# Kernel tuning notes

Measured on AMD Instinct MI355X. Metric: run time of the kernel, lower is better.

The kernel has to match this reference:

```python
import jax, jax.numpy as jnp
from jax import lax
import numpy as np


def _bn(x, g, b, eps=1e-5):
    # BatchNorm2d in training mode: biased batch stats over (N,H,W) per channel
    m = jnp.mean(x, axis=(0, 2, 3), keepdims=True)
    v = jnp.mean((x - m) ** 2, axis=(0, 2, 3), keepdims=True)
    return (x - m) * lax.rsqrt(v + eps) * g[None, :, None, None] + b[None, :, None, None]


def _conv(x, w, b, pad):
    y = lax.conv_general_dilated(x, w, (1, 1), [(pad, pad), (pad, pad)],
                                 dimension_numbers=('NCHW', 'OIHW', 'NCHW'))
    return y + b[None, :, None, None]


def _prelu(x, a):
    return jnp.where(x >= 0, x, a * x)


def _maxpool2(x):
    return lax.reduce_window(x, -jnp.inf, lax.max, (1, 1, 2, 2), (1, 1, 2, 2), 'VALID')


def _up2(x):
    # UpsamplingBilinear2d(scale_factor=2) -> bilinear, align_corners=True
    B, C, H, W = x.shape
    def idx(n):
        pos = jnp.arange(2 * n, dtype=x.dtype) * (n - 1) / (2 * n - 1)
        lo = jnp.floor(pos).astype(jnp.int32)
        hi = jnp.minimum(lo + 1, n - 1)
        return lo, hi, pos - lo.astype(x.dtype)
    lo, hi, f = idx(H)
    x = x[:, :, lo, :] * (1 - f)[:, None] + x[:, :, hi, :] * f[:, None]
    lo, hi, f = idx(W)
    x = x[:, :, :, lo] * (1 - f) + x[:, :, :, hi] * f
    return x


def _forward(x, n16, sigma16, bias16, prelu_a,
             bn3_g, bn3_b, bn32_g, bn32_b, bn64_g, bn64_b, bn128_g, bn128_b,
             w1, b1, w2, b2, w3, b3, w4, b4, w5, b5, w6, b6, w7, b7, w11, b11):
    B, C, H, W = x.shape
    # 16 enhancement curves fused: r_k = x^{n_k} / (x^{n_k} + sigma_k^{n_k} + bias_k)
    xn = x[None] ** n16[:, None, None, None, None]          # (16,B,3,H,W)
    r = xn / (xn + (sigma16 ** n16)[:, None, None, None, None]
              + bias16[:, None, None, None, None])
    # each branch gets its own BatchNorm2d(3) stats (same affine params)
    r = jax.vmap(lambda t: _bn(t, bn3_g, bn3_b))(r)
    x_fusion = jnp.transpose(r, (1, 0, 2, 3, 4)).reshape(B, 16 * C, H, W)
    x1 = _bn(_maxpool2(_prelu(_conv(x_fusion, w1, b1, 1), prelu_a)), bn32_g, bn32_b)
    x2 = _bn(_maxpool2(_prelu(_conv(x1, w2, b2, 1), prelu_a)), bn64_g, bn64_b)
    x3 = _bn(_maxpool2(_prelu(_conv(x2, w3, b3, 1), prelu_a)), bn128_g, bn128_b)
    x4 = _bn(_conv(x3, w4, b4, 1), bn128_g, bn128_b)
    x5 = _bn(_up2(_prelu(_conv(jnp.concatenate([x4, x3], 1), w5, b5, 1), prelu_a)), bn64_g, bn64_b)
    x6 = _bn(_up2(_prelu(_conv(jnp.concatenate([x2, x5], 1), w6, b6, 1), prelu_a)), bn32_g, bn32_b)
    x_out = jax.nn.sigmoid(_up2(_prelu(_conv(jnp.concatenate([x1, x6], 1), w7, b7, 1), prelu_a)))
    x_out = _conv(x_out, w11, b11, 0)
    x_mean = jnp.mean(x, axis=1, keepdims=True)
    x_out1 = jnp.mean(x_out, axis=1, keepdims=True)
    return x_out1 * (x / (x_mean + 1e-6))


def setup_inputs() -> dict:
    key = jax.random.key(0)
    ks = jax.random.split(key, 16)
    B, H, W = 8, 256, 256
    nf = 32
    x = jax.random.uniform(ks[0], (B, 3, H, W), jnp.float32, 1e-3, 1.0)
    n16 = jnp.arange(1, 17, dtype=jnp.float32) * 0.5
    sigma16 = jnp.full((16,), 0.5, jnp.float32)
    bias16 = jnp.full((16,), 1e-4, jnp.float32)
    prelu_a = jnp.float32(0.25)
    def cw(k, o, i, kk):
        return jax.random.normal(k, (o, i, kk, kk), jnp.float32) * 0.05
    def cb(o):
        return jnp.zeros((o,), jnp.float32)
    return dict(
        x=x, n16=n16, sigma16=sigma16, bias16=bias16, prelu_a=prelu_a,
        bn3_g=jnp.ones((3,), jnp.float32), bn3_b=jnp.zeros((3,), jnp.float32),
        bn32_g=jnp.ones((32,), jnp.float32), bn32_b=jnp.zeros((32,), jnp.float32),
        bn64_g=jnp.ones((64,), jnp.float32), bn64_b=jnp.zeros((64,), jnp.float32),
        bn128_g=jnp.ones((128,), jnp.float32), bn128_b=jnp.zeros((128,), jnp.float32),
        w1=cw(ks[1], nf, 48, 3), b1=cb(nf),
        w2=cw(ks[2], 2 * nf, nf, 3), b2=cb(2 * nf),
        w3=cw(ks[3], 4 * nf, 2 * nf, 3), b3=cb(4 * nf),
        w4=cw(ks[4], 4 * nf, 4 * nf, 3), b4=cb(4 * nf),
        w5=cw(ks[5], 2 * nf, 8 * nf, 3), b5=cb(2 * nf),
        w6=cw(ks[6], nf, 4 * nf, 3), b6=cb(nf),
        w7=cw(ks[7], nf, 2 * nf, 3), b7=cb(nf),
        w11=cw(ks[8], 3, nf, 1), b11=cb(3),
    )


def reference(x, n16, sigma16, bias16, prelu_a,
              bn3_g, bn3_b, bn32_g, bn32_b, bn64_g, bn64_b, bn128_g, bn128_b,
              w1, b1, w2, b2, w3, b3, w4, b4, w5, b5, w6, b6, w7, b7, w11, b11):
    return _forward(x, n16, sigma16, bias16, prelu_a,
                    bn3_g, bn3_b, bn32_g, bn32_b, bn64_g, bn64_b, bn128_g, bn128_b,
                    w1, b1, w2, b2, w3, b3, w4, b4, w5, b5, w6, b6, w7, b7, w11, b11)
```

## Files before the change

kernel.cpp:

```cpp
#include <hip/hip_runtime.h>

#define FAST_EXP2(x) __builtin_amdgcn_exp2f(x)
#define FAST_LOG2(x) __builtin_amdgcn_logf(x)
#define FAST_RCP(x)  __builtin_amdgcn_rcpf(x)

static constexpr size_t S3_SUM=0,   S3_SQ=48;
static constexpr size_t S32A_SUM=96,  S32A_SQ=128;
static constexpr size_t S64A_SUM=160, S64A_SQ=224;
static constexpr size_t S128A_SUM=288,S128A_SQ=416;
static constexpr size_t S128B_SUM=544,S128B_SQ=672;
static constexpr size_t S64B_SUM=800, S64B_SQ=864;
static constexpr size_t S32B_SUM=928, S32B_SQ=960;
static constexpr size_t A3_=1024,  B3_=1072;
static constexpr size_t A32A_=1120, B32A_=1152;
static constexpr size_t A64A_=1184, B64A_=1248;
static constexpr size_t A128A_=1312,B128A_=1440;
static constexpr size_t A128B_=1568,B128B_=1696;
static constexpr size_t A64B_=1824, B64B_=1888;
static constexpr size_t A32B_=1952, B32B_=1984;
static constexpr size_t SPB_=2016, WBAR_=2032, BBAR_=2064;
static constexpr size_t XF_=4096;
static constexpr size_t T1_=XF_+25165824;
static constexpr size_t T2_=T1_+4194304;
static constexpr size_t T3_=T2_+2097152;
static constexpr size_t T4_=T3_+1048576;
static constexpr size_t C5_=T4_+1048576;
static constexpr size_t U5_=C5_+524288;
static constexpr size_t C6_=U5_+2097152;
static constexpr size_t U6_=C6_+1048576;
static constexpr size_t C7_=U6_+4194304;

__global__ void k_precomp(const float* __restrict__ n16, const float* __restrict__ sig16,
                          const float* __restrict__ b16, const float* __restrict__ w11,
                          const float* __restrict__ b11,
                          float* __restrict__ spb, float* __restrict__ wbar, float* __restrict__ bbar)
{
    int t = threadIdx.x;
    if (t < 16) spb[t] = powf(sig16[t], n16[t]) + b16[t];
    else if (t < 48) { int j = t - 16; wbar[j] = (w11[j] + w11[32 + j] + w11[64 + j]) * (1.f/3.f); }
    else if (t == 48) bbar[0] = (b11[0] + b11[1] + b11[2]) * (1.f/3.f);
}

__global__ __launch_bounds__(256) void k_branch_stats(
    const float* __restrict__ x, const float* __restrict__ n16,
    const float* __restrict__ sig16, const float* __restrict__ b16,
    float* __restrict__ sum, float* __restrict__ sq)
{
    const int c = blockIdx.x >> 6;
    const int chunk = blockIdx.x & 63;
    float nk[16], den[16];
#pragma unroll
    for (int k = 0; k < 16; ++k) { nk[k] = n16[k]; den[k] = powf(sig16[k], nk[k]) + b16[k]; }
    float s[16], q[16];
#pragma unroll
    for (int k = 0; k < 16; ++k) { s[k] = 0.f; q[k] = 0.f; }
    const int per = 8192;
    int start = chunk * per;
    for (int i = start + (int)threadIdx.x; i < start + per; i += 256) {
        int b = i >> 16, hw = i & 65535;
        float xv = x[(size_t)(b*3 + c)*65536 + hw];
        float t = FAST_LOG2(xv);
#pragma unroll
        for (int k = 0; k < 16; ++k) {
            float v = FAST_EXP2(nk[k]*t);
            float r = v * FAST_RCP(v + den[k]);
            s[k] += r; q[k] += r*r;
        }
    }
    __shared__ float red[4][32];
    int lane = threadIdx.x & 63, wid = threadIdx.x >> 6;
#pragma unroll
    for (int k = 0; k < 16; ++k) {
#pragma unroll
        for (int off = 32; off > 0; off >>= 1) {
            s[k] += __shfl_down(s[k], off);
            q[k] += __shfl_down(q[k], off);
        }
    }
    if (lane == 0) {
#pragma unroll
        for (int k = 0; k < 16; ++k) { red[wid][k] = s[k]; red[wid][16+k] = q[k]; }
    }
    __syncthreads();
    if (threadIdx.x < 32) {
        float v = red[0][threadIdx.x] + red[1][threadIdx.x] + red[2][threadIdx.x] + red[3][threadIdx.x];
        int k = threadIdx.x & 15;
        if (threadIdx.x < 16) atomicAdd(&sum[k*3 + c], v);
        else                  atomicAdd(&sq[k*3 + c], v);
    }
}

__global__ __launch_bounds__(256) void k_stats(
    const float* __restrict__ in, int C, int HW, int nchunks, int per,
    float* __restrict__ sum, float* __restrict__ sq)
{
    int c = blockIdx.x / nchunks;
    int chunk = blockIdx.x - c*nchunks;
    float s = 0.f, q = 0.f;
    int start = chunk * per, end = start + per;
    for (int i = start + (int)threadIdx.x; i < end; i += 256) {
        int b = i / HW, hw = i - b*HW;
        float v = in[((size_t)b*C + c)*HW + hw];
        s += v; q += v*v;
    }
#pragma unroll
    for (int off = 32; off > 0; off >>= 1) { s += __shfl_down(s, off); q += __shfl_down(q, off); }
    __shared__ float ss[4], qq[4];
    int lane = threadIdx.x & 63, wid = threadIdx.x >> 6;
    if (lane == 0) { ss[wid] = s; qq[wid] = q; }
    __syncthreads();
    if (threadIdx.x == 0) {
        atomicAdd(&sum[c], ss[0]+ss[1]+ss[2]+ss[3]);
        atomicAdd(&sq[c],  qq[0]+qq[1]+qq[2]+qq[3]);
    }
}

__global__ void k_finalize(const float* __restrict__ sum, const float* __restrict__ sq,
                           const float* __restrict__ g, const float* __restrict__ bb,
                           int C, int gdim, float invN,
                           float* __restrict__ A, float* __restrict__ Bs)
{
    int i = blockIdx.x*blockDim.x + threadIdx.x;
    if (i < C) {
        float m   = sum[i]*invN;
        float var = fmaxf(sq[i]*invN - m*m, 0.f);
        float inv = rsqrtf(var + 1e-5f);
        float a   = g[i % gdim]*inv;
        A[i]  = a;
        Bs[i] = bb[i % gdim] - m*a;
    }
}

__global__ __launch_bounds__(256) void k_fusion(
    const float* __restrict__ x, const float* __restrict__ n16, const float* __restrict__ spb,
    const float* __restrict__ A, const float* __restrict__ Bs, float* __restrict__ out)
{
    int idx = blockIdx.x*256 + threadIdx.x;
    if (idx >= 8*3*65536) return;
    int hw = idx & 65535;
    int bc = idx >> 16;
    int b = bc / 3, c = bc - b*3;
    float xv = x[idx];
    float t = FAST_LOG2(xv);
    size_t obase = ((size_t)b*48 + c)*65536 + hw;
#pragma unroll
    for (int k = 0; k < 16; ++k) {
        float v = FAST_EXP2(n16[k]*t);
        float r = v * FAST_RCP(v + spb[k]);
        int ch = k*3 + c;
        out[obase + (size_t)(k*3)*65536] = r*A[ch] + Bs[ch];
    }
}

__global__ __launch_bounds__(256) void k_fill(
    float* __restrict__ out, const float* __restrict__ bias, int C, int HW, int total)
{
    int idx = blockIdx.x*256 + threadIdx.x;
    if (idx < total) {
        int c = (idx / HW) % C;
        out[idx] = bias[c];
    }
}

template<int COG, int CHUNK>
__global__ __launch_bounds__(256) void k_cpool(
    const float* __restrict__ in, int Cin,
    const float* __restrict__ sc, const float* __restrict__ sh,
    const float* __restrict__ w, const float* __restrict__ bias,
    int Cout, int H, int W, const float* __restrict__ prelu_a,
    float* __restrict__ out)
{
    const int Hp = H >> 1, Wp = W >> 1;
    const int tx = threadIdx.x & 15, ty = threadIdx.x >> 4;
    const int nco = Cout / COG;
    const int b = blockIdx.z / nco, cob = (blockIdx.z - b*nco)*COG;
    const int x0 = blockIdx.x*32, y0 = blockIdx.y*32;
    __shared__ float tile[CHUNK][34*36];
    float acc[COG][4];
#pragma unroll
    for (int i = 0; i < COG; ++i)
#pragma unroll
        for (int j = 0; j < 4; ++j) acc[i][j] = 0.f;

#pragma unroll 1
    for (int cb = 0; cb < Cin; cb += CHUNK) {
#pragma unroll
        for (int sub = 0; sub < CHUNK; ++sub) {
            int ci = cb + sub;
            float scv = sc ? sc[ci] : 1.f;
            float shv = sc ? sh[ci] : 0.f;
            const float* base = in + ((size_t)b*Cin + ci)*H*W;
#pragma unroll 1
            for (int i = threadIdx.x; i < 1156; i += 256) {
                int r = i / 34, c = i - r*34;
                int gy = y0 - 1 + r, gx = x0 - 1 + c;
                float v = 0.f;
                if ((unsigned)gy < (unsigned)H && (unsigned)gx < (unsigned)W)
                    v = base[(size_t)gy*W + gx]*scv + shv;
                tile[sub][r*36 + c] = v;
            }
        }
        __syncthreads();
#pragma unroll
        for (int sub = 0; sub < CHUNK; ++sub) {
            const float* tl = &tile[sub][(2*ty)*36 + 2*tx];
            float iv[4][4];
#pragma unroll
            for (int r = 0; r < 4; ++r)
#pragma unroll
                for (int c = 0; c < 4; ++c) iv[r][c] = tl[r*36 + c];
#pragma unroll
            for (int co = 0; co < COG; ++co) {
                const float* wp = w + (((size_t)(cob+co))*Cin + cb + sub)*9;
#pragma unroll
                for (int kh = 0; kh < 3; ++kh)
#pragma unroll
                    for (int kw = 0; kw < 3; ++kw) {
                        float wv = wp[kh*3 + kw];
                        acc[co][0] += wv*iv[kh+0][kw+0];
                        acc[co][1] += wv*iv[kh+0][kw+1];
                        acc[co][2] += wv*iv[kh+1][kw+0];
                        acc[co][3] += wv*iv[kh+1][kw+1];
                    }
            }
        }
        __syncthreads();
    }
    float a = __ldg(prelu_a);
    int py = blockIdx.y*16 + ty, px = blockIdx.x*16 + tx;
#pragma unroll
    for (int co = 0; co < COG; ++co) {
        float bv = bias[cob + co];
        float m = -INFINITY;
#pragma unroll
        for (int p = 0; p < 4; ++p) {
            float v = acc[co][p] + bv;
            v = v >= 0.f ? v : a*v;
            m = fmaxf(m, v);
        }
        out[(((size_t)b*Cout + cob + co)*Hp + py)*Wp + px] = m;
    }
}

template<int COG, int CHUNK, bool STORE>
__global__ __launch_bounds__(256) void k_csplit(
    const float* __restrict__ in1, int C1,
    const float* __restrict__ sc1, const float* __restrict__ sh1,
    const float* __restrict__ in2, int C2,
    const float* __restrict__ sc2, const float* __restrict__ sh2,
    const float* __restrict__ w, const float* __restrict__ bias,
    int Cout, int H, int W, const float* __restrict__ prelu_a, int do_prelu,
    int ciN, int nsplit,
    float* __restrict__ out)
{
    const int tx = threadIdx.x & 15, ty = threadIdx.x >> 4;
    const int nco = Cout / COG;
    int z = blockIdx.z;
    const int sp = z % nsplit; z /= nsplit;
    const int b = z / nco, cob = (z - b*nco)*COG;
    const int ci0 = sp * ciN;
    const int x0 = blockIdx.x*32, y0 = blockIdx.y*32;
    const int Cin = C1 + C2;
    __shared__ float tile[CHUNK][34*36];
    float acc[COG][4];
#pragma unroll
    for (int i = 0; i < COG; ++i)
#pragma unroll
        for (int j = 0; j < 4; ++j) acc[i][j] = 0.f;

#pragma unroll 1
    for (int cb = 0; cb < ciN; cb += CHUNK) {
#pragma unroll
        for (int sub = 0; sub < CHUNK; ++sub) {
            int ci = ci0 + cb + sub;
            const float* in; int cc; const float* scp; const float* shp; int Cn;
            if (ci < C1) { in = in1; cc = ci;      scp = sc1; shp = sh1; Cn = C1; }
            else         { in = in2; cc = ci - C1; scp = sc2; shp = sh2; Cn = C2; }
            float scv = scp ? scp[cc] : 1.f;
            float shv = scp ? shp[cc] : 0.f;
            const float* base = in + ((size_t)b*Cn + cc)*H*W;
#pragma unroll 1
            for (int i = threadIdx.x; i < 1156; i += 256) {
                int r = i / 34, c = i - r*34;
                int gy = y0 - 1 + r, gx = x0 - 1 + c;
                float v = 0.f;
                if ((unsigned)gy < (unsigned)H && (unsigned)gx < (unsigned)W)
                    v = base[(size_t)gy*W + gx]*scv + shv;
                tile[sub][r*36 + c] = v;
            }
        }
        __syncthreads();
#pragma unroll
        for (int sub = 0; sub < CHUNK; ++sub) {
            const float* tl = &tile[sub][(2*ty)*36 + 2*tx];
            float iv[4][4];
#pragma unroll
            for (int r = 0; r < 4; ++r)
#pragma unroll
                for (int c = 0; c < 4; ++c) iv[r][c] = tl[r*36 + c];
#pragma unroll
            for (int co = 0; co < COG; ++co) {
                const float* wp = w + (((size_t)(cob+co))*Cin + ci0 + cb + sub)*9;
#pragma unroll
                for (int kh = 0; kh < 3; ++kh)
#pragma unroll
                    for (int kw = 0; kw < 3; ++kw) {
                        float wv = wp[kh*3 + kw];
                        acc[co][0] += wv*iv[kh+0][kw+0];
                        acc[co][1] += wv*iv[kh+0][kw+1];
                        acc[co][2] += wv*iv[kh+1][kw+0];
                        acc[co][3] += wv*iv[kh+1][kw+1];
                    }
            }
        }
        __syncthreads();
    }
    int oy = y0 + 2*ty, ox = x0 + 2*tx;
    if (STORE) {
        float a = __ldg(prelu_a);
#pragma unroll
        for (int co = 0; co < COG; ++co) {
            float bv = bias[cob + co];
            float* op = out + (((size_t)b*Cout + cob + co)*H + oy)*W + ox;
#pragma unroll
            for (int p = 0; p < 4; ++p) {
                float v = acc[co][p] + bv;
                if (do_prelu) v = v >= 0.f ? v : a*v;
                op[(p>>1)*W + (p&1)] = v;
            }
        }
    } else {
#pragma unroll
        for (int co = 0; co < COG; ++co) {
            float* op = out + (((size_t)b*Cout + cob + co)*H + oy)*W + ox;
#pragma unroll
            for (int p = 0; p < 4; ++p)
                atomicAdd(&op[(p>>1)*W + (p&1)], acc[co][p]);
        }
    }
}

__global__ __launch_bounds__(256) void k_up2(
    const float* __restrict__ in, float* __restrict__ out, int BC, int h, int w,
    const float* __restrict__ prelu_a, int do_prelu)
{
    int idx = blockIdx.x*256 + threadIdx.x;
    int W2 = 2*w, H2 = 2*h;
    int total = BC*H2*W2;
    if (idx >= total) return;
    float a = do_prelu ? __ldg(prelu_a) : 0.f;
    int ox = idx % W2; int t = idx / W2; int oy = t % H2; int bc = t / H2;
    float py = ((float)oy * (float)(h-1)) / (float)(2*h - 1);
    int ly = (int)floorf(py); int hy = min(ly+1, h-1); float fy = py - (float)ly;
    float px = ((float)ox * (float)(w-1)) / (float)(2*w - 1);
    int lx = (int)floorf(px); int hx = min(lx+1, w-1); float fx = px - (float)lx;
    const float* p = in + (size_t)bc*h*w;
    float v00 = p[(size_t)ly*w + lx], v01 = p[(size_t)ly*w + hx];
    float v10 = p[(size_t)hy*w + lx], v11 = p[(size_t)hy*w + hx];
    if (do_prelu) {
        v00 = v00 >= 0.f ? v00 : a*v00;
        v01 = v01 >= 0.f ? v01 : a*v01;
        v10 = v10 >= 0.f ? v10 : a*v10;
        v11 = v11 >= 0.f ? v11 : a*v11;
    }
    float v0 = v00*(1.f-fx) + v01*fx;
    float v1 = v10*(1.f-fx) + v11*fx;
    out[idx] = v0*(1.f-fy) + v1*fy;
}

__global__ __launch_bounds__(256) void k_final(
    const float* __restrict__ c7, const float* __restrict__ x,
    const float* __restrict__ wbar, const float* __restrict__ bbar,
    float* __restrict__ out)
{
    int idx = blockIdx.x*256 + threadIdx.x;
    if (idx >= 8*65536) return;
    int hw = idx & 65535, b = idx >> 16;
    int oy = hw >> 8, ox = hw & 255;
    float py = ((float)oy * 127.f) / 255.f;
    int ly = (int)floorf(py); int hy = min(ly+1, 127); float fy = py - (float)ly;
    float px = ((float)ox * 127.f) / 255.f;
    int lx = (int)floorf(px); int hx = min(lx+1, 127); float fx = px - (float)lx;
    float w00 = (1.f-fy)*(1.f-fx), w01 = (1.f-fy)*fx, w10 = fy*(1.f-fx), w11v = fy*fx;
    const float* base = c7 + (size_t)b*32*16384;
    float accum = bbar[0];
#pragma unroll 8
    for (int j = 0; j < 32; ++j) {
        const float* p = base + (size_t)j*16384;
        float v = p[ly*128 + lx]*w00 + p[ly*128 + hx]*w01 + p[hy*128 + lx]*w10 + p[hy*128 + hx]*w11v;
        float s = FAST_RCP(1.f + __expf(-v));
        accum += wbar[j]*s;
    }
    size_t xb = (size_t)b*3*65536 + hw;
    float x0 = x[xb], x1 = x[xb + 65536], x2 = x[xb + 2*65536];
    float m = (x0 + x1 + x2)*(1.f/3.f) + 1e-6f;
    float sc = accum * FAST_RCP(m);
    out[xb]            = sc*x0;
    out[xb + 65536]    = sc*x1;
    out[xb + 2*65536]  = sc*x2;
}

extern "C" void kernel_launch(void* const* d_in, const int* in_sizes, int n_in,
                              void* d_out, int out_size, void* d_ws, size_t ws_size,
                              hipStream_t stream) {
    const float* x       = (const float*)d_in[0];
    const float* n16     = (const float*)d_in[1];
    const float* sig16   = (const float*)d_in[2];
    const float* bia16   = (const float*)d_in[3];
    const float* prelu_a = (const float*)d_in[4];
    const float* bn3_g   = (const float*)d_in[5];
    const float* bn3_b   = (const float*)d_in[6];
    const float* bn32_g  = (const float*)d_in[7];
    const float* bn32_b  = (const float*)d_in[8];
    const float* bn64_g  = (const float*)d_in[9];
    const float* bn64_b  = (const float*)d_in[10];
    const float* bn128_g = (const float*)d_in[11];
    const float* bn128_b = (const float*)d_in[12];
    const float* w1 = (const float*)d_in[13]; const float* b1 = (const float*)d_in[14];
    const float* w2 = (const float*)d_in[15]; const float* b2 = (const float*)d_in[16];
    const float* w3 = (const float*)d_in[17]; const float* b3 = (const float*)d_in[18];
    const float* w4 = (const float*)d_in[19]; const float* b4 = (const float*)d_in[20];
    const float* w5 = (const float*)d_in[21]; const float* b5 = (const float*)d_in[22];
    const float* w6 = (const float*)d_in[23]; const float* b6 = (const float*)d_in[24];
    const float* w7 = (const float*)d_in[25]; const float* b7 = (const float*)d_in[26];
    const float* w11= (const float*)d_in[27]; const float* b11= (const float*)d_in[28];
    float* ws  = (float*)d_ws;
    float* out = (float*)d_out;

    (void)hipMemsetAsync(d_ws, 0, 4096*sizeof(float), stream);

    k_precomp<<<1, 64, 0, stream>>>(n16, sig16, bia16, w11, b11, ws+SPB_, ws+WBAR_, ws+BBAR_);

    k_branch_stats<<<192, 256, 0, stream>>>(x, n16, sig16, bia16, ws+S3_SUM, ws+S3_SQ);
    k_finalize<<<1, 128, 0, stream>>>(ws+S3_SUM, ws+S3_SQ, bn3_g, bn3_b, 48, 3, 1.f/524288.f, ws+A3_, ws+B3_);
    k_fusion<<<6144, 256, 0, stream>>>(x, n16, ws+SPB_, ws+A3_, ws+B3_, ws+XF_);

    k_cpool<16,4><<<dim3(8,8,16), 256, 0, stream>>>(ws+XF_, 48, nullptr, nullptr,
                                                    w1, b1, 32, 256, 256, prelu_a, ws+T1_);
    k_stats<<<2048, 256, 0, stream>>>(ws+T1_, 32, 16384, 64, 2048, ws+S32A_SUM, ws+S32A_SQ);
    k_finalize<<<1, 128, 0, stream>>>(ws+S32A_SUM, ws+S32A_SQ, bn32_g, bn32_b, 32, 32, 1.f/131072.f, ws+A32A_, ws+B32A_);

    k_cpool<8,4><<<dim3(4,4,64), 256, 0, stream>>>(ws+T1_, 32, ws+A32A_, ws+B32A_,
                                                   w2, b2, 64, 128, 128, prelu_a, ws+T2_);
    k_stats<<<1024, 256, 0, stream>>>(ws+T2_, 64, 4096, 16, 2048, ws+S64A_SUM, ws+S64A_SQ);
    k_finalize<<<1, 128, 0, stream>>>(ws+S64A_SUM, ws+S64A_SQ, bn64_g, bn64_b, 64, 64, 1.f/32768.f, ws+A64A_, ws+B64A_);

    k_cpool<8,4><<<dim3(2,2,128), 256, 0, stream>>>(ws+T2_, 64, ws+A64A_, ws+B64A_,
                                                    w3, b3, 128, 64, 64, prelu_a, ws+T3_);
    k_stats<<<512, 256, 0, stream>>>(ws+T3_, 128, 1024, 4, 2048, ws+S128A_SUM, ws+S128A_SQ);
    k_finalize<<<1, 128, 0, stream>>>(ws+S128A_SUM, ws+S128A_SQ, bn128_g, bn128_b, 128, 128, 1.f/8192.f, ws+A128A_, ws+B128A_);

    k_fill<<<4096, 256, 0, stream>>>(ws+T4_, b4, 128, 1024, 1048576);
    k_csplit<8,4,false><<<dim3(1,1,512), 256, 0, stream>>>(ws+T3_, 128, ws+A128A_, ws+B128A_,
                                                           nullptr, 0, nullptr, nullptr,
                                                           w4, nullptr, 128, 32, 32, prelu_a, 0,
                                                           32, 4, ws+T4_);
    k_stats<<<512, 256, 0, stream>>>(ws+T4_, 128, 1024, 4, 2048, ws+S128B_SUM, ws+S128B_SQ);
    k_finalize<<<1, 128, 0, stream>>>(ws+S128B_SUM, ws+S128B_SQ, bn128_g, bn128_b, 128, 128, 1.f/8192.f, ws+A128B_, ws+B128B_);

    k_fill<<<2048, 256, 0, stream>>>(ws+C5_, b5, 64, 1024, 524288);
    k_csplit<8,4,false><<<dim3(1,1,512), 256, 0, stream>>>(ws+T4_, 128, ws+A128B_, ws+B128B_,
                                                           ws+T3_, 128, ws+A128A_, ws+B128A_,
                                                           w5, nullptr, 64, 32, 32, prelu_a, 0,
                                                           32, 8, ws+C5_);
    k_up2<<<8192, 256, 0, stream>>>(ws+C5_, ws+U5_, 8*64, 32, 32, prelu_a, 1);
    k_stats<<<1024, 256, 0, stream>>>(ws+U5_, 64, 4096, 16, 2048, ws+S64B_SUM, ws+S64B_SQ);
    k_finalize<<<1, 128, 0, stream>>>(ws+S64B_SUM, ws+S64B_SQ, bn64_g, bn64_b, 64, 64, 1.f/32768.f, ws+A64B_, ws+B64B_);

    k_fill<<<4096, 256, 0, stream>>>(ws+C6_, b6, 32, 4096, 1048576);
    k_csplit<8,4,false><<<dim3(2,2,128), 256, 0, stream>>>(ws+T2_, 64, ws+A64A_, ws+B64A_,
                                                           ws+U5_, 64, ws+A64B_, ws+B64B_,
                                                           w6, nullptr, 32, 64, 64, prelu_a, 0,
                                                           32, 4, ws+C6_);
    k_up2<<<16384, 256, 0, stream>>>(ws+C6_, ws+U6_, 8*32, 64, 64, prelu_a, 1);
    k_stats<<<2048, 256, 0, stream>>>(ws+U6_, 32, 16384, 64, 2048, ws+S32B_SUM, ws+S32B_SQ);
    k_finalize<<<1, 128, 0, stream>>>(ws+S32B_SUM, ws+S32B_SQ, bn32_g, bn32_b, 32, 32, 1.f/131072.f, ws+A32B_, ws+B32B_);

    k_csplit<8,4,true><<<dim3(4,4,32), 256, 0, stream>>>(ws+T1_, 32, ws+A32A_, ws+B32A_,
                                                         ws+U6_, 32, ws+A32B_, ws+B32B_,
                                                         w7, b7, 32, 128, 128, prelu_a, 1,
                                                         64, 1, ws+C7_);

    k_final<<<2048, 256, 0, stream>>>(ws+C7_, x, ws+WBAR_, ws+BBAR_, out);
}
```

Before: 1.685 ms.

## Stage conv weights in shared memory and widen per-thread output tiles

Replaces the pooled conv and split conv kernels with two new kernels. Both stage the block's weight slice in LDS in a co-innermost layout so weights come in as float4. The large-resolution convs now use 64-wide tiles with a 2x4 output patch per thread and vectorized LDS input reads, which raises arithmetic reuse per load. Output-channel groups and launch grids are retuned, and occupancy hints are added; the trade-off is more registers per thread and more LDS per block.

```diff
diff --git a/kernel.cpp b/kernel.cpp
--- a/kernel.cpp
+++ b/kernel.cpp
@@ -162,97 +162,145 @@
     }
 }
 
-template<int COG, int CHUNK>
-__global__ __launch_bounds__(256) void k_cpool(
-    const float* __restrict__ in, int Cin,
-    const float* __restrict__ sc, const float* __restrict__ sh,
-    const float* __restrict__ w, const float* __restrict__ bias,
-    int Cout, int H, int W, const float* __restrict__ prelu_a,
-    float* __restrict__ out)
-{
-    const int Hp = H >> 1, Wp = W >> 1;
-    const int tx = threadIdx.x & 15, ty = threadIdx.x >> 4;
-    const int nco = Cout / COG;
-    const int b = blockIdx.z / nco, cob = (blockIdx.z - b*nco)*COG;
-    const int x0 = blockIdx.x*32, y0 = blockIdx.y*32;
-    __shared__ float tile[CHUNK][34*36];
-    float acc[COG][4];
-#pragma unroll
-    for (int i = 0; i < COG; ++i)
-#pragma unroll
-        for (int j = 0; j < 4; ++j) acc[i][j] = 0.f;
-
-#pragma unroll 1
-    for (int cb = 0; cb < Cin; cb += CHUNK) {
-#pragma unroll
-        for (int sub = 0; sub < CHUNK; ++sub) {
-            int ci = cb + sub;
-            float scv = sc ? sc[ci] : 1.f;
-            float shv = sc ? sh[ci] : 0.f;
-            const float* base = in + ((size_t)b*Cin + ci)*H*W;
-#pragma unroll 1
-            for (int i = threadIdx.x; i < 1156; i += 256) {
-                int r = i / 34, c = i - r*34;
-                int gy = y0 - 1 + r, gx = x0 - 1 + c;
-                float v = 0.f;
-                if ((unsigned)gy < (unsigned)H && (unsigned)gx < (unsigned)W)
-                    v = base[(size_t)gy*W + gx]*scv + shv;
-                tile[sub][r*36 + c] = v;
-            }
-        }
-        __syncthreads();
-#pragma unroll
-        for (int sub = 0; sub < CHUNK; ++sub) {
-            const float* tl = &tile[sub][(2*ty)*36 + 2*tx];
-            float iv[4][4];
-#pragma unroll
-            for (int r = 0; r < 4; ++r)
-#pragma unroll
-                for (int c = 0; c < 4; ++c) iv[r][c] = tl[r*36 + c];
-#pragma unroll
-            for (int co = 0; co < COG; ++co) {
-                const float* wp = w + (((size_t)(cob+co))*Cin + cb + sub)*9;
-#pragma unroll
-                for (int kh = 0; kh < 3; ++kh)
-#pragma unroll
-                    for (int kw = 0; kw < 3; ++kw) {
-                        float wv = wp[kh*3 + kw];
-                        acc[co][0] += wv*iv[kh+0][kw+0];
-                        acc[co][1] += wv*iv[kh+0][kw+1];
-                        acc[co][2] += wv*iv[kh+1][kw+0];
-                        acc[co][3] += wv*iv[kh+1][kw+1];
-                    }
-            }
-        }
-        __syncthreads();
-    }
-    float a = __ldg(prelu_a);
-    int py = blockIdx.y*16 + ty, px = blockIdx.x*16 + tx;
-#pragma unroll
-    for (int co = 0; co < COG; ++co) {
-        float bv = bias[cob + co];
-        float m = -INFINITY;
-#pragma unroll
-        for (int p = 0; p < 4; ++p) {
-            float v = acc[co][p] + bv;
-            v = v >= 0.f ? v : a*v;
-            m = fmaxf(m, v);
-        }
-        out[(((size_t)b*Cout + cob + co)*Hp + py)*Wp + px] = m;
-    }
-}
-
-template<int COG, int CHUNK, bool STORE>
-__global__ __launch_bounds__(256) void k_csplit(
+template<int COG, bool POOL>
+__global__ __launch_bounds__(256,4) void k_conv_big(
     const float* __restrict__ in1, int C1,
     const float* __restrict__ sc1, const float* __restrict__ sh1,
     const float* __restrict__ in2, int C2,
     const float* __restrict__ sc2, const float* __restrict__ sh2,
     const float* __restrict__ w, const float* __restrict__ bias,
     int Cout, int H, int W, const float* __restrict__ prelu_a, int do_prelu,
-    int ciN, int nsplit,
     float* __restrict__ out)
 {
+    const int Cin = C1 + C2;
+    const int tx = threadIdx.x & 15, ty = threadIdx.x >> 4;
+    const int nco = Cout / COG;
+    const int b = blockIdx.z / nco, cob = (blockIdx.z - b*nco)*COG;
+    const int x0 = blockIdx.x*64, y0 = blockIdx.y*32;
+
+    __shared__ float wl[COG*64*9];
+    __shared__ float tile[2][34*68];
+
+    for (int t = threadIdx.x; t < COG*Cin*9; t += 256) {
+        int co = t % COG; int rest = t / COG;
+        int k = rest % 9; int ci = rest / 9;
+        wl[t] = w[(((size_t)(cob+co))*Cin + ci)*9 + k];
+    }
+
+    float acc[COG][8];
+#pragma unroll
+    for (int i = 0; i < COG; ++i)
+#pragma unroll
+        for (int j = 0; j < 8; ++j) acc[i][j] = 0.f;
+
+#pragma unroll 1
+    for (int cb = 0; cb < Cin; cb += 2) {
+#pragma unroll
+        for (int sub = 0; sub < 2; ++sub) {
+            int ci = cb + sub;
+            const float* in; int cc; const float* scp; const float* shp; int Cn;
+            if (ci < C1) { in = in1; cc = ci;      scp = sc1; shp = sh1; Cn = C1; }
+            else         { in = in2; cc = ci - C1; scp = sc2; shp = sh2; Cn = C2; }
+            float scv = scp ? scp[cc] : 1.f;
+            float shv = scp ? shp[cc] : 0.f;
+            const float* base = in + ((size_t)b*Cn + cc)*H*W;
+#pragma unroll 1
+            for (int i = threadIdx.x; i < 34*66; i += 256) {
+                int r = i / 66, c = i - r*66;
+                int gy = y0 - 1 + r, gx = x0 - 1 + c;
+                float v = 0.f;
+                if ((unsigned)gy < (unsigned)H && (unsigned)gx < (unsigned)W)
+                    v = base[(size_t)gy*W + gx]*scv + shv;
+                tile[sub][r*68 + c] = v;
+            }
+        }
+        __syncthreads();
+#pragma unroll
+        for (int sub = 0; sub < 2; ++sub) {
+            const float* tl = &tile[sub][(2*ty)*68 + 4*tx];
+            float iv[4][6];
+#pragma unroll
+            for (int r = 0; r < 4; ++r) {
+                float4 av = *(const float4*)(tl + r*68);
+                float2 bv = *(const float2*)(tl + r*68 + 4);
+                iv[r][0]=av.x; iv[r][1]=av.y; iv[r][2]=av.z; iv[r][3]=av.w;
+                iv[r][4]=bv.x; iv[r][5]=bv.y;
+            }
+            const float* wbase = &wl[(cb+sub)*9*COG];
+#pragma unroll
+            for (int kh = 0; kh < 3; ++kh)
+#pragma unroll
+            for (int kw = 0; kw < 3; ++kw) {
+                const int k = kh*3 + kw;
+                float wv[COG];
+#pragma unroll
+                for (int q = 0; q < COG/4; ++q) {
+                    float4 wq = *((const float4*)(wbase + k*COG) + q);
+                    wv[4*q+0]=wq.x; wv[4*q+1]=wq.y; wv[4*q+2]=wq.z; wv[4*q+3]=wq.w;
+                }
+#pragma unroll
+                for (int co = 0; co < COG; ++co)
+#pragma unroll
+                    for (int py = 0; py < 2; ++py)
+#pragma unroll
+                        for (int px = 0; px < 4; ++px)
+                            acc[co][py*4+px] += wv[co]*iv[py+kh][px+kw];
+            }
+        }
+        __syncthreads();
+    }
+
+    float a = __ldg(prelu_a);
+    if (POOL) {
+        const int Hp = H >> 1, Wp = W >> 1;
+        int pyp = (y0 >> 1) + ty, pxp = (x0 >> 1) + 2*tx;
+#pragma unroll
+        for (int co = 0; co < COG; ++co) {
+            float bv = bias[cob + co];
+            float v[8];
+#pragma unroll
+            for (int p = 0; p < 8; ++p) {
+                float t = acc[co][p] + bv;
+                v[p] = t >= 0.f ? t : a*t;
+            }
+            float2 st;
+            st.x = fmaxf(fmaxf(v[0], v[1]), fmaxf(v[4], v[5]));
+            st.y = fmaxf(fmaxf(v[2], v[3]), fmaxf(v[6], v[7]));
+            *(float2*)(out + (((size_t)b*Cout + cob + co)*Hp + pyp)*Wp + pxp) = st;
+        }
+    } else {
+        int oy = y0 + 2*ty, ox = x0 + 4*tx;
+#pragma unroll
+        for (int co = 0; co < COG; ++co) {
+            float bv = bias[cob + co];
+            float* op = out + (((size_t)b*Cout + cob + co)*H + oy)*W + ox;
+#pragma unroll
+            for (int py = 0; py < 2; ++py) {
+                float4 st;
+                float t0 = acc[co][py*4+0] + bv, t1 = acc[co][py*4+1] + bv;
+                float t2 = acc[co][py*4+2] + bv, t3 = acc[co][py*4+3] + bv;
+                if (do_prelu) {
+                    t0 = t0 >= 0.f ? t0 : a*t0; t1 = t1 >= 0.f ? t1 : a*t1;
+                    t2 = t2 >= 0.f ? t2 : a*t2; t3 = t3 >= 0.f ? t3 : a*t3;
+                }
+                st.x=t0; st.y=t1; st.z=t2; st.w=t3;
+                *(float4*)(op + py*W) = st;
+            }
+        }
+    }
+}
+
+template<int COG>
+__global__ __launch_bounds__(256,4) void k_conv_sm(
+    const float* __restrict__ in1, int C1,
+    const float* __restrict__ sc1, const float* __restrict__ sh1,
+    const float* __restrict__ in2, int C2,
+    const float* __restrict__ sc2, const float* __restrict__ sh2,
+    const float* __restrict__ w,
+    int Cout, int H, int W, int ciN, int nsplit,
+    float* __restrict__ out)
+{
+    const int Cin = C1 + C2;
     const int tx = threadIdx.x & 15, ty = threadIdx.x >> 4;
     const int nco = Cout / COG;
     int z = blockIdx.z;
@@ -260,8 +308,16 @@
     const int b = z / nco, cob = (z - b*nco)*COG;
     const int ci0 = sp * ciN;
     const int x0 = blockIdx.x*32, y0 = blockIdx.y*32;
-    const int Cin = C1 + C2;
-    __shared__ float tile[CHUNK][34*36];
+
+    __shared__ float wl[COG*32*9];
+    __shared__ float tile[2][34*36];
+
+    for (int t = threadIdx.x; t < COG*ciN*9; t += 256) {
+        int co = t % COG; int rest = t / COG;
+        int k = rest % 9; int ci = rest / 9;
+        wl[t] = w[(((size_t)(cob+co))*Cin + ci0 + ci)*9 + k];
+    }
+
     float acc[COG][4];
 #pragma unroll
     for (int i = 0; i < COG; ++i)
@@ -269,9 +325,9 @@
         for (int j = 0; j < 4; ++j) acc[i][j] = 0.f;
 
 #pragma unroll 1
-    for (int cb = 0; cb < ciN; cb += CHUNK) {
-#pragma unroll
-        for (int sub = 0; sub < CHUNK; ++sub) {
+    for (int cb = 0; cb < ciN; cb += 2) {
+#pragma unroll
+        for (int sub = 0; sub < 2; ++sub) {
             int ci = ci0 + cb + sub;
             const float* in; int cc; const float* scp; const float* shp; int Cn;
             if (ci < C1) { in = in1; cc = ci;      scp = sc1; shp = sh1; Cn = C1; }
@@ -280,7 +336,7 @@
             float shv = scp ? shp[cc] : 0.f;
             const float* base = in + ((size_t)b*Cn + cc)*H*W;
 #pragma unroll 1
-            for (int i = threadIdx.x; i < 1156; i += 256) {
+            for (int i = threadIdx.x; i < 34*34; i += 256) {
                 int r = i / 34, c = i - r*34;
                 int gy = y0 - 1 + r, gx = x0 - 1 + c;
                 float v = 0.f;
@@ -291,52 +347,47 @@
         }
         __syncthreads();
 #pragma unroll
-        for (int sub = 0; sub < CHUNK; ++sub) {
+        for (int sub = 0; sub < 2; ++sub) {
             const float* tl = &tile[sub][(2*ty)*36 + 2*tx];
             float iv[4][4];
 #pragma unroll
-            for (int r = 0; r < 4; ++r)
-#pragma unroll
-                for (int c = 0; c < 4; ++c) iv[r][c] = tl[r*36 + c];
-#pragma unroll
-            for (int co = 0; co < COG; ++co) {
-                const float* wp = w + (((size_t)(cob+co))*Cin + ci0 + cb + sub)*9;
-#pragma unroll
-                for (int kh = 0; kh < 3; ++kh)
-#pragma unroll
-                    for (int kw = 0; kw < 3; ++kw) {
-                        float wv = wp[kh*3 + kw];
-                        acc[co][0] += wv*iv[kh+0][kw+0];
-                        acc[co][1] += wv*iv[kh+0][kw+1];
-                        acc[co][2] += wv*iv[kh+1][kw+0];
-                        acc[co][3] += wv*iv[kh+1][kw+1];
-                    }
+            for (int r = 0; r < 4; ++r) {
+                float2 a2 = *(const float2*)(tl + r*36);
+                float2 b2 = *(const float2*)(tl + r*36 + 2);
+                iv[r][0]=a2.x; iv[r][1]=a2.y; iv[r][2]=b2.x; iv[r][3]=b2.y;
+            }
+            const float* wbase = &wl[(cb+sub)*9*COG];
+#pragma unroll
+            for (int kh = 0; kh < 3; ++kh)
+#pragma unroll
+            for (int kw = 0; kw < 3; ++kw) {
+                const int k = kh*3 + kw;
+                float wv[COG];
+#pragma unroll
+                for (int q = 0; q < COG/4; ++q) {
+                    float4 wq = *((const float4*)(wbase + k*COG) + q);
+                    wv[4*q+0]=wq.x; wv[4*q+1]=wq.y; wv[4*q+2]=wq.z; wv[4*q+3]=wq.w;
+                }
+#pragma unroll
+                for (int co = 0; co < COG; ++co)
+#pragma unroll
+                    for (int py = 0; py < 2; ++py)
+#pragma unroll
+                        for (int px = 0; px < 2; ++px)
+                            acc[co][py*2+px] += wv[co]*iv[py+kh][px+kw];
             }
         }
         __syncthreads();
     }
+
     int oy = y0 + 2*ty, ox = x0 + 2*tx;
-    if (STORE) {
-        float a = __ldg(prelu_a);
-#pragma unroll
-        for (int co = 0; co < COG; ++co) {
-            float bv = bias[cob + co];
-            float* op = out + (((size_t)b*Cout + cob + co)*H + oy)*W + ox;
-#pragma unroll
-            for (int p = 0; p < 4; ++p) {
-                float v = acc[co][p] + bv;
-                if (do_prelu) v = v >= 0.f ? v : a*v;
-                op[(p>>1)*W + (p&1)] = v;
-            }
-        }
-    } else {
-#pragma unroll
-        for (int co = 0; co < COG; ++co) {
-            float* op = out + (((size_t)b*Cout + cob + co)*H + oy)*W + ox;
-#pragma unroll
-            for (int p = 0; p < 4; ++p)
-                atomicAdd(&op[(p>>1)*W + (p&1)], acc[co][p]);
-        }
+#pragma unroll
+    for (int co = 0; co < COG; ++co) {
+        float* op = out + (((size_t)b*Cout + cob + co)*H + oy)*W + ox;
+        atomicAdd(&op[0],     acc[co][0]);
+        atomicAdd(&op[1],     acc[co][1]);
+        atomicAdd(&op[W],     acc[co][2]);
+        atomicAdd(&op[W + 1], acc[co][3]);
     }
 }
 
@@ -435,51 +486,50 @@
     k_finalize<<<1, 128, 0, stream>>>(ws+S3_SUM, ws+S3_SQ, bn3_g, bn3_b, 48, 3, 1.f/524288.f, ws+A3_, ws+B3_);
     k_fusion<<<6144, 256, 0, stream>>>(x, n16, ws+SPB_, ws+A3_, ws+B3_, ws+XF_);
 
-    k_cpool<16,4><<<dim3(8,8,16), 256, 0, stream>>>(ws+XF_, 48, nullptr, nullptr,
-                                                    w1, b1, 32, 256, 256, prelu_a, ws+T1_);
+    k_conv_big<8,true><<<dim3(4,8,32), 256, 0, stream>>>(
+        ws+XF_, 48, nullptr, nullptr, nullptr, 0, nullptr, nullptr,
+        w1, b1, 32, 256, 256, prelu_a, 1, ws+T1_);
     k_stats<<<2048, 256, 0, stream>>>(ws+T1_, 32, 16384, 64, 2048, ws+S32A_SUM, ws+S32A_SQ);
     k_finalize<<<1, 128, 0, stream>>>(ws+S32A_SUM, ws+S32A_SQ, bn32_g, bn32_b, 32, 32, 1.f/131072.f, ws+A32A_, ws+B32A_);
 
-    k_cpool<8,4><<<dim3(4,4,64), 256, 0, stream>>>(ws+T1_, 32, ws+A32A_, ws+B32A_,
-                                                   w2, b2, 64, 128, 128, prelu_a, ws+T2_);
+    k_conv_big<4,true><<<dim3(2,4,128), 256, 0, stream>>>(
+        ws+T1_, 32, ws+A32A_, ws+B32A_, nullptr, 0, nullptr, nullptr,
+        w2, b2, 64, 128, 128, prelu_a, 1, ws+T2_);
     k_stats<<<1024, 256, 0, stream>>>(ws+T2_, 64, 4096, 16, 2048, ws+S64A_SUM, ws+S64A_SQ);
     k_finalize<<<1, 128, 0, stream>>>(ws+S64A_SUM, ws+S64A_SQ, bn64_g, bn64_b, 64, 64, 1.f/32768.f, ws+A64A_, ws+B64A_);
 
-    k_cpool<8,4><<<dim3(2,2,128), 256, 0, stream>>>(ws+T2_, 64, ws+A64A_, ws+B64A_,
-                                                    w3, b3, 128, 64, 64, prelu_a, ws+T3_);
+    k_conv_big<4,true><<<dim3(1,2,256), 256, 0, stream>>>(
+        ws+T2_, 64, ws+A64A_, ws+B64A_, nullptr, 0, nullptr, nullptr,
+        w3, b3, 128, 64, 64, prelu_a, 1, ws+T3_);
     k_stats<<<512, 256, 0, stream>>>(ws+T3_, 128, 1024, 4, 2048, ws+S128A_SUM, ws+S128A_SQ);
     k_finalize<<<1, 128, 0, stream>>>(ws+S128A_SUM, ws+S128A_SQ, bn128_g, bn128_b, 128, 128, 1.f/8192.f, ws+A128A_, ws+B128A_);
 
     k_fill<<<4096, 256, 0, stream>>>(ws+T4_, b4, 128, 1024, 1048576);
-    k_csplit<8,4,false><<<dim3(1,1,512), 256, 0, stream>>>(ws+T3_, 128, ws+A128A_, ws+B128A_,
-                                                           nullptr, 0, nullptr, nullptr,
-                                                           w4, nullptr, 128, 32, 32, prelu_a, 0,
-                                                           32, 4, ws+T4_);
+    k_conv_sm<8><<<dim3(1,1,512), 256, 0, stream>>>(
+        ws+T3_, 128, ws+A128A_, ws+B128A_, nullptr, 0, nullptr, nullptr,
+        w4, 128, 32, 32, 32, 4, ws+T4_);
     k_stats<<<512, 256, 0, stream>>>(ws+T4_, 128, 1024, 4, 2048, ws+S128B_SUM, ws+S128B_SQ);
     k_finalize<<<1, 128, 0, stream>>>(ws+S128B_SUM, ws+S128B_SQ, bn128_g, bn128_b, 128, 128, 1.f/8192.f, ws+A128B_, ws+B128B_);
 
     k_fill<<<2048, 256, 0, stream>>>(ws+C5_, b5, 64, 1024, 524288);
-    k_csplit<8,4,false><<<dim3(1,1,512), 256, 0, stream>>>(ws+T4_, 128, ws+A128B_, ws+B128B_,
-                                                           ws+T3_, 128, ws+A128A_, ws+B128A_,
-                                                           w5, nullptr, 64, 32, 32, prelu_a, 0,
-                                                           32, 8, ws+C5_);
+    k_conv_sm<8><<<dim3(1,1,512), 256, 0, stream>>>(
+        ws+T4_, 128, ws+A128B_, ws+B128B_, ws+T3_, 128, ws+A128A_, ws+B128A_,
+        w5, 64, 32, 32, 32, 8, ws+C5_);
     k_up2<<<8192, 256, 0, stream>>>(ws+C5_, ws+U5_, 8*64, 32, 32, prelu_a, 1);
     k_stats<<<1024, 256, 0, stream>>>(ws+U5_, 64, 4096, 16, 2048, ws+S64B_SUM, ws+S64B_SQ);
     k_finalize<<<1, 128, 0, stream>>>(ws+S64B_SUM, ws+S64B_SQ, bn64_g, bn64_b, 64, 64, 1.f/32768.f, ws+A64B_, ws+B64B_);
 
     k_fill<<<4096, 256, 0, stream>>>(ws+C6_, b6, 32, 4096, 1048576);
-    k_csplit<8,4,false><<<dim3(2,2,128), 256, 0, stream>>>(ws+T2_, 64, ws+A64A_, ws+B64A_,
-                                                           ws+U5_, 64, ws+A64B_, ws+B64B_,
-                                                           w6, nullptr, 32, 64, 64, prelu_a, 0,
-                                                           32, 4, ws+C6_);
+    k_conv_sm<8><<<dim3(2,2,128), 256, 0, stream>>>(
+        ws+T2_, 64, ws+A64A_, ws+B64A_, ws+U5_, 64, ws+A64B_, ws+B64B_,
+        w6, 32, 64, 64, 32, 4, ws+C6_);
     k_up2<<<16384, 256, 0, stream>>>(ws+C6_, ws+U6_, 8*32, 64, 64, prelu_a, 1);
     k_stats<<<2048, 256, 0, stream>>>(ws+U6_, 32, 16384, 64, 2048, ws+S32B_SUM, ws+S32B_SQ);
     k_finalize<<<1, 128, 0, stream>>>(ws+S32B_SUM, ws+S32B_SQ, bn32_g, bn32_b, 32, 32, 1.f/131072.f, ws+A32B_, ws+B32B_);
 
-    k_csplit<8,4,true><<<dim3(4,4,32), 256, 0, stream>>>(ws+T1_, 32, ws+A32A_, ws+B32A_,
-                                                         ws+U6_, 32, ws+A32B_, ws+B32B_,
-                                                         w7, b7, 32, 128, 128, prelu_a, 1,
-                                                         64, 1, ws+C7_);
+    k_conv_big<4,false><<<dim3(2,4,64), 256, 0, stream>>>(
+        ws+T1_, 32, ws+A32A_, ws+B32A_, ws+U6_, 32, ws+A32B_, ws+B32B_,
+        w7, b7, 32, 128, 128, prelu_a, 1, ws+C7_);
 
     k_final<<<2048, 256, 0, stream>>>(ws+C7_, x, ws+WBAR_, ws+BBAR_, out);
 }
```

New measurement: 1.684 ms. Within noise of the previous version (-0.1%).
